# Kernel tuning notes

Hardware: AMD Instinct MI355X
Metric: run time of the kernel (lower is better)

The kernel has to match this reference:

```python
import jax, jax.numpy as jnp
import numpy as np

NIN, NHID, NDECHID, NOUT = 128, 256, 512, 10
B, N = 32, 4096


def _linear_params(key, fan_in, fan_out):
    kw, kb = jax.random.split(key)
    bound = 1.0 / np.sqrt(fan_in)
    W = jax.random.uniform(kw, (fan_in, fan_out), jnp.float32, -bound, bound)
    b = jax.random.uniform(kb, (fan_out,), jnp.float32, -bound, bound)
    return W, b


def setup_inputs() -> dict:
    key = jax.random.key(0)
    ks = jax.random.split(key, 7)
    x = jax.random.normal(ks[0], (B, N, NIN), jnp.float32)
    W1, b1 = _linear_params(ks[1], NIN, NHID)
    W2, b2 = _linear_params(ks[2], NHID, NHID)
    W3, b3 = _linear_params(ks[3], NHID, NHID)
    D1, c1 = _linear_params(ks[4], NHID, NDECHID)
    D2, c2 = _linear_params(ks[5], NDECHID, NDECHID)
    D3, c3 = _linear_params(ks[6], NDECHID, NOUT)
    return {"x": x, "W1": W1, "b1": b1, "W2": W2, "b2": b2, "W3": W3, "b3": b3,
            "D1": D1, "c1": c1, "D2": D2, "c2": c2, "D3": D3, "c3": c3}


def reference(x, W1, b1, W2, b2, W3, b3, D1, c1, D2, c2, D3, c3):
    # encoder MLP: Linear-ReLU-Linear-ReLU-Linear, then extra ReLU
    h = jax.nn.relu(x @ W1 + b1)            # [B, N, nhid]
    h = jax.nn.relu(h @ W2 + b2)
    h = jax.nn.relu(h @ W3 + b3)            # fused enc output + F.relu
    # mean_{i,j}(h_i * h_j) over the set == (mean_i h)^2 elementwise (exact identity)
    m = jnp.mean(h, axis=1)                  # [B, nhid]
    p = jax.nn.relu(m * m)                   # [B, nhid]
    # decoder MLP
    d = jax.nn.relu(p @ D1 + c1)
    d = jax.nn.relu(d @ D2 + c2)
    return d @ D3 + c3                       # [B, nout]
```

## Files before the change

kernel.cpp:

```cpp
#include <hip/hip_runtime.h>
#include <hip/hip_bf16.h>
#include <stdint.h>


#define NIN   128
#define NHID  256
#define NDEC  512
#define NOUTC 10
#define BATCH 32
#define NTOK  4096
#define MTILE 64
#define NBLK  (BATCH * (NTOK / MTILE))

#define SWZ(t) (((t) & 7) << 4)

typedef short bf16x8 __attribute__((ext_vector_type(8)));
typedef float floatx4 __attribute__((ext_vector_type(4)));

__device__ __forceinline__ uint16_t f2b(float f) {
  union { uint32_t u; float f; } v; v.f = f;
  uint32_t r = v.u + 0x7FFFu + ((v.u >> 16) & 1u);
  return (uint16_t)(r >> 16);
}
__device__ __forceinline__ uint32_t pkbf(float lo, float hi) {
  __hip_bfloat162 h = __float22bfloat162_rn(float2{lo, hi});
  union { __hip_bfloat162 h; uint32_t u; } c; c.h = h;
  return c.u;
}

__global__ __launch_bounds__(256) void pack_weights(
    const float* __restrict__ W1, const float* __restrict__ W2,
    const float* __restrict__ W3, const float* __restrict__ c3,
    uint8_t* __restrict__ pW, float* __restrict__ msum,
    float* __restrict__ out) {
  int p = blockIdx.x * blockDim.x + threadIdx.x;
  if (p < BATCH * NHID) msum[p] = 0.f;
  if (p < BATCH * NOUTC) out[p] = c3[p % NOUTC];
  if (p < 32768) {
    int j = p & 7, ln = (p >> 3) & 63, rest = p >> 9;
    int kc = rest & 3, mt = rest >> 2;
    int m = mt * 16 + (ln & 15);
    int k = kc * 32 + ((ln >> 4) << 3) + j;
    ((uint16_t*)pW)[p] = f2b(W1[k * NHID + m]);
  } else {
    int p2 = p - 32768;
    const float* W = (p2 < 65536) ? W2 : W3;
    int base = (p2 < 65536) ? 65536 : 131072;
    if (p2 >= 65536) p2 -= 65536;
    int j = p2 & 7, ln = (p2 >> 3) & 63, rest = p2 >> 9;
    int kc = rest & 7, mt = rest >> 3;
    int m = mt * 16 + (ln & 15);
    int k = kc * 32 + ((ln >> 4) << 3) + j;
    int r = __builtin_amdgcn_cvt_pk_fp8_f32(W[k * NHID + m], 0.f, 0, false);
    pW[base + p2] = (uint8_t)(r & 0xFF);
  }
}

__global__ __launch_bounds__(512) void encoder(
    const float* __restrict__ x,
    const uint8_t* __restrict__ pW,
    const float* __restrict__ b1,
    const float* __restrict__ b2,
    const float* __restrict__ b3,
    float* __restrict__ msum) {
  __shared__ __align__(16) uint8_t Hs[MTILE * 256];
  __shared__ __align__(16) float scr[NHID];

  const int tid  = threadIdx.x;
  const int wave = tid >> 6;
  const int lane = tid & 63;
  const int l15  = lane & 15;
  const int q    = lane >> 4;
  const int tok0  = blockIdx.x * MTILE;
  const int batch = blockIdx.x >> 6;

  const uint16_t* pW1 = (const uint16_t*)pW;
  const uint8_t*  pW2 = pW + 65536;
  const uint8_t*  pW3 = pW + 131072;

  {
    const float4* xv = (const float4*)(x + (size_t)tok0 * NIN);
#pragma unroll
    for (int i = 0; i < 2; ++i) {
      const int u = tid + i * 512;
      float4 va = xv[2 * u];
      float4 vb = xv[2 * u + 1];
      uint4 w = make_uint4(pkbf(va.x, va.y), pkbf(va.z, va.w),
                           pkbf(vb.x, vb.y), pkbf(vb.z, vb.w));
      const int row = u >> 4;
      const int cb  = (u & 15) << 4;
      *(uint4*)&Hs[row * 256 + (cb ^ SWZ(row))] = w;
    }
  }
  __syncthreads();

  floatx4 acc[2][4];

#pragma unroll
  for (int jt = 0; jt < 2; ++jt) {
    const float4 bb = *(const float4*)&b1[(wave * 2 + jt) * 16 + q * 4];
#pragma unroll
    for (int tt = 0; tt < 4; ++tt)
      acc[jt][tt] = (floatx4){bb.x, bb.y, bb.z, bb.w};
  }
#pragma unroll
  for (int kc = 0; kc < 4; ++kc) {
    bf16x8 a0 = *(const bf16x8*)(pW1 + ((((wave * 2 + 0) * 4 + kc) * 64 + lane) << 3));
    bf16x8 a1 = *(const bf16x8*)(pW1 + ((((wave * 2 + 1) * 4 + kc) * 64 + lane) << 3));
#pragma unroll
    for (int tt = 0; tt < 4; ++tt) {
      const int t = tt * 16 + l15;
      bf16x8 b = *(const bf16x8*)&Hs[t * 256 + ((kc * 64 + q * 16) ^ SWZ(t))];
      acc[0][tt] = __builtin_amdgcn_mfma_f32_16x16x32_bf16(a0, b, acc[0][tt], 0, 0, 0);
      acc[1][tt] = __builtin_amdgcn_mfma_f32_16x16x32_bf16(a1, b, acc[1][tt], 0, 0, 0);
    }
  }
  __syncthreads();

#pragma unroll
  for (int jt = 0; jt < 2; ++jt) {
    const int j0 = (wave * 2 + jt) * 16 + q * 4;
#pragma unroll
    for (int tt = 0; tt < 4; ++tt) {
      const int t = tt * 16 + l15;
      float v0 = fmaxf(acc[jt][tt][0], 0.f);
      float v1 = fmaxf(acc[jt][tt][1], 0.f);
      float v2 = fmaxf(acc[jt][tt][2], 0.f);
      float v3 = fmaxf(acc[jt][tt][3], 0.f);
      int u = __builtin_amdgcn_cvt_pk_fp8_f32(v0, v1, 0, false);
      u = __builtin_amdgcn_cvt_pk_fp8_f32(v2, v3, u, true);
      *(uint32_t*)&Hs[t * 256 + (j0 ^ SWZ(t))] = (uint32_t)u;
    }
  }
  __syncthreads();

#pragma unroll
  for (int jt = 0; jt < 2; ++jt) {
    const float4 bb = *(const float4*)&b2[(wave * 2 + jt) * 16 + q * 4];
#pragma unroll
    for (int tt = 0; tt < 4; ++tt)
      acc[jt][tt] = (floatx4){bb.x, bb.y, bb.z, bb.w};
  }
#pragma unroll
  for (int kc = 0; kc < 8; ++kc) {
    long a0 = *(const long*)(pW2 + ((((wave * 2 + 0) * 8 + kc) * 64 + lane) << 3));
    long a1 = *(const long*)(pW2 + ((((wave * 2 + 1) * 8 + kc) * 64 + lane) << 3));
#pragma unroll
    for (int tt = 0; tt < 4; ++tt) {
      const int t = tt * 16 + l15;
      long b = *(const long*)&Hs[t * 256 + ((kc * 32 + q * 8) ^ SWZ(t))];
      acc[0][tt] = __builtin_amdgcn_mfma_f32_16x16x32_fp8_fp8(a0, b, acc[0][tt], 0, 0, 0);
      acc[1][tt] = __builtin_amdgcn_mfma_f32_16x16x32_fp8_fp8(a1, b, acc[1][tt], 0, 0, 0);
    }
  }
  __syncthreads();

#pragma unroll
  for (int jt = 0; jt < 2; ++jt) {
    const int j0 = (wave * 2 + jt) * 16 + q * 4;
#pragma unroll
    for (int tt = 0; tt < 4; ++tt) {
      const int t = tt * 16 + l15;
      float v0 = fmaxf(acc[jt][tt][0], 0.f);
      float v1 = fmaxf(acc[jt][tt][1], 0.f);
      float v2 = fmaxf(acc[jt][tt][2], 0.f);
      float v3 = fmaxf(acc[jt][tt][3], 0.f);
      int u = __builtin_amdgcn_cvt_pk_fp8_f32(v0, v1, 0, false);
      u = __builtin_amdgcn_cvt_pk_fp8_f32(v2, v3, u, true);
      *(uint32_t*)&Hs[t * 256 + (j0 ^ SWZ(t))] = (uint32_t)u;
    }
  }
  __syncthreads();

#pragma unroll
  for (int jt = 0; jt < 2; ++jt) {
    const float4 bb = *(const float4*)&b3[(wave * 2 + jt) * 16 + q * 4];
#pragma unroll
    for (int tt = 0; tt < 4; ++tt)
      acc[jt][tt] = (floatx4){bb.x, bb.y, bb.z, bb.w};
  }
#pragma unroll
  for (int kc = 0; kc < 8; ++kc) {
    long a0 = *(const long*)(pW3 + ((((wave * 2 + 0) * 8 + kc) * 64 + lane) << 3));
    long a1 = *(const long*)(pW3 + ((((wave * 2 + 1) * 8 + kc) * 64 + lane) << 3));
#pragma unroll
    for (int tt = 0; tt < 4; ++tt) {
      const int t = tt * 16 + l15;
      long b = *(const long*)&Hs[t * 256 + ((kc * 32 + q * 8) ^ SWZ(t))];
      acc[0][tt] = __builtin_amdgcn_mfma_f32_16x16x32_fp8_fp8(a0, b, acc[0][tt], 0, 0, 0);
      acc[1][tt] = __builtin_amdgcn_mfma_f32_16x16x32_fp8_fp8(a1, b, acc[1][tt], 0, 0, 0);
    }
  }

#pragma unroll
  for (int jt = 0; jt < 2; ++jt) {
    float s0 = 0.f, s1 = 0.f, s2 = 0.f, s3 = 0.f;
#pragma unroll
    for (int tt = 0; tt < 4; ++tt) {
      s0 += fmaxf(acc[jt][tt][0], 0.f);
      s1 += fmaxf(acc[jt][tt][1], 0.f);
      s2 += fmaxf(acc[jt][tt][2], 0.f);
      s3 += fmaxf(acc[jt][tt][3], 0.f);
    }
#pragma unroll
    for (int m = 1; m <= 8; m <<= 1) {
      s0 += __shfl_xor(s0, m);
      s1 += __shfl_xor(s1, m);
      s2 += __shfl_xor(s2, m);
      s3 += __shfl_xor(s3, m);
    }
    if (l15 == 0)
      *(float4*)&scr[(wave * 2 + jt) * 16 + q * 4] = (float4){s0, s1, s2, s3};
  }
  __syncthreads();
  if (tid < NHID)
    atomicAdd(&msum[batch * NHID + tid], scr[tid]);
}

__global__ __launch_bounds__(1024) void decoder(
    const float* __restrict__ msum,
    const float* __restrict__ D1, const float* __restrict__ c1,
    const float* __restrict__ D2, const float* __restrict__ c2,
    const float* __restrict__ D3,
    float* __restrict__ out) {
  __shared__ float p[NHID];
  __shared__ float d1[NDEC];
  __shared__ float d2q[128];
  __shared__ __align__(16) float red[4096];
  const int b = blockIdx.x >> 2, qd = blockIdx.x & 3, t = threadIdx.x;

  if (t < NHID) {
    float m = msum[b * NHID + t] * (1.f / NTOK);
    p[t] = m * m;
  }
  __syncthreads();

  {
    const int jg = t & 127;
    const int ks = t >> 7;
    const float4* D1v = (const float4*)D1;
    float4 s = {0.f, 0.f, 0.f, 0.f};
    for (int k = ks * 32; k < ks * 32 + 32; ++k) {
      float4 w = D1v[k * 128 + jg];
      float pv = p[k];
      s.x += pv * w.x; s.y += pv * w.y; s.z += pv * w.z; s.w += pv * w.w;
    }
    *(float4*)&red[t * 4] = s;
    __syncthreads();
    if (t < NDEC) {
      float v = c1[t];
#pragma unroll
      for (int i = 0; i < 8; ++i) v += red[i * 512 + t];
      d1[t] = fmaxf(v, 0.f);
    }
    __syncthreads();
  }

  {
    const int jg2 = t & 31;
    const int ks2 = t >> 5;
    const float4* D2v = (const float4*)D2;
    float4 s = {0.f, 0.f, 0.f, 0.f};
    for (int k = ks2 * 16; k < ks2 * 16 + 16; ++k) {
      float4 w = D2v[k * 128 + qd * 32 + jg2];
      float hv = d1[k];
      s.x += hv * w.x; s.y += hv * w.y; s.z += hv * w.z; s.w += hv * w.w;
    }
    *(float4*)&red[t * 4] = s;
    __syncthreads();
    if (t < 128) {
      float v = c2[qd * 128 + t];
#pragma unroll
      for (int i = 0; i < 32; ++i) v += red[i * 128 + t];
      d2q[t] = fmaxf(v, 0.f);
    }
    __syncthreads();
  }

  {
    const int j3 = t & 15;
    const int kc = t >> 4;
    float s = 0.f;
    if (j3 < NOUTC)
      for (int k = kc * 2; k < kc * 2 + 2; ++k)
        s += d2q[k] * D3[(qd * 128 + k) * NOUTC + j3];
    red[t] = s;
    __syncthreads();
    if (t < NOUTC) {
      float v = 0.f;
#pragma unroll
      for (int i = 0; i < 64; ++i) v += red[i * 16 + t];
      atomicAdd(&out[b * NOUTC + t], v);
    }
  }
}

extern "C" void kernel_launch(void* const* d_in, const int* in_sizes, int n_in,
                              void* d_out, int out_size, void* d_ws, size_t ws_size,
                              hipStream_t stream) {
  const float* x  = (const float*)d_in[0];
  const float* W1 = (const float*)d_in[1];
  const float* b1 = (const float*)d_in[2];
  const float* W2 = (const float*)d_in[3];
  const float* b2 = (const float*)d_in[4];
  const float* W3 = (const float*)d_in[5];
  const float* b3 = (const float*)d_in[6];
  const float* D1 = (const float*)d_in[7];
  const float* c1 = (const float*)d_in[8];
  const float* D2 = (const float*)d_in[9];
  const float* c2 = (const float*)d_in[10];
  const float* D3 = (const float*)d_in[11];
  const float* c3 = (const float*)d_in[12];

  uint8_t* pW   = (uint8_t*)d_ws;
  float*   msum = (float*)((char*)d_ws + 384 * 1024);

  pack_weights<<<640, 256, 0, stream>>>(W1, W2, W3, c3, pW, msum,
                                        (float*)d_out);
  encoder<<<NBLK, 512, 0, stream>>>(x, pW, b1, b2, b3, msum);
  decoder<<<128, 1024, 0, stream>>>(msum, D1, c1, D2, c2, D3,
                                    (float*)d_out);
}
```

Baseline: 157.9 us.

## Double-buffer activation tiles and permute fp8 layout for 16-byte LDS reads

Splits the shared activation buffer into two ping-pong buffers so each layer writes its output into the buffer not being read, which lets one __syncthreads per layer transition be removed. The fp8 activations are also stored in a permuted column order with a wider XOR swizzle, so each lane fetches two k-chunks with one 16-byte LDS load instead of two 8-byte loads. This doubles the LDS footprint per block, which may reduce occupancy, and correctness depends on the permuted layout matching the MFMA k ordering.

Result: no change. 155.1 us (-1.7%).

```diff
diff --git a/kernel.cpp b/kernel.cpp
--- a/kernel.cpp
+++ b/kernel.cpp
@@ -12,10 +12,11 @@
 #define MTILE 64
 #define NBLK  (BATCH * (NTOK / MTILE))
 
-#define SWZ(t) (((t) & 7) << 4)
+#define SW2(t) (((t) & 15) << 4)
 
 typedef short bf16x8 __attribute__((ext_vector_type(8)));
 typedef float floatx4 __attribute__((ext_vector_type(4)));
+typedef long  longx2  __attribute__((ext_vector_type(2)));
 
 __device__ __forceinline__ uint16_t f2b(float f) {
   union { uint32_t u; float f; } v; v.f = f;
@@ -63,7 +64,8 @@
     const float* __restrict__ b2,
     const float* __restrict__ b3,
     float* __restrict__ msum) {
-  __shared__ __align__(16) uint8_t Hs[MTILE * 256];
+  __shared__ __align__(16) uint8_t Hs0[MTILE * 256];
+  __shared__ __align__(16) uint8_t Hs1[MTILE * 256];
   __shared__ __align__(16) float scr[NHID];
 
   const int tid  = threadIdx.x;
@@ -89,7 +91,7 @@
                            pkbf(vb.x, vb.y), pkbf(vb.z, vb.w));
       const int row = u >> 4;
       const int cb  = (u & 15) << 4;
-      *(uint4*)&Hs[row * 256 + (cb ^ SWZ(row))] = w;
+      *(uint4*)&Hs0[row * 256 + (cb ^ SW2(row))] = w;
     }
   }
   __syncthreads();
@@ -110,16 +112,15 @@
 #pragma unroll
     for (int tt = 0; tt < 4; ++tt) {
       const int t = tt * 16 + l15;
-      bf16x8 b = *(const bf16x8*)&Hs[t * 256 + ((kc * 64 + q * 16) ^ SWZ(t))];
+      bf16x8 b = *(const bf16x8*)&Hs0[t * 256 + ((kc * 64 + q * 16) ^ SW2(t))];
       acc[0][tt] = __builtin_amdgcn_mfma_f32_16x16x32_bf16(a0, b, acc[0][tt], 0, 0, 0);
       acc[1][tt] = __builtin_amdgcn_mfma_f32_16x16x32_bf16(a1, b, acc[1][tt], 0, 0, 0);
     }
   }
-  __syncthreads();
-
 #pragma unroll
   for (int jt = 0; jt < 2; ++jt) {
     const int j0 = (wave * 2 + jt) * 16 + q * 4;
+    const int pb = ((j0 >> 3) & 3) * 64 + (j0 >> 5) * 8 + (j0 & 7);
 #pragma unroll
     for (int tt = 0; tt < 4; ++tt) {
       const int t = tt * 16 + l15;
@@ -129,7 +130,7 @@
       float v3 = fmaxf(acc[jt][tt][3], 0.f);
       int u = __builtin_amdgcn_cvt_pk_fp8_f32(v0, v1, 0, false);
       u = __builtin_amdgcn_cvt_pk_fp8_f32(v2, v3, u, true);
-      *(uint32_t*)&Hs[t * 256 + (j0 ^ SWZ(t))] = (uint32_t)u;
+      *(uint32_t*)&Hs1[t * 256 + (pb ^ SW2(t))] = (uint32_t)u;
     }
   }
   __syncthreads();
@@ -142,22 +143,29 @@
       acc[jt][tt] = (floatx4){bb.x, bb.y, bb.z, bb.w};
   }
 #pragma unroll
-  for (int kc = 0; kc < 8; ++kc) {
-    long a0 = *(const long*)(pW2 + ((((wave * 2 + 0) * 8 + kc) * 64 + lane) << 3));
-    long a1 = *(const long*)(pW2 + ((((wave * 2 + 1) * 8 + kc) * 64 + lane) << 3));
-#pragma unroll
-    for (int tt = 0; tt < 4; ++tt) {
-      const int t = tt * 16 + l15;
-      long b = *(const long*)&Hs[t * 256 + ((kc * 32 + q * 8) ^ SWZ(t))];
-      acc[0][tt] = __builtin_amdgcn_mfma_f32_16x16x32_fp8_fp8(a0, b, acc[0][tt], 0, 0, 0);
-      acc[1][tt] = __builtin_amdgcn_mfma_f32_16x16x32_fp8_fp8(a1, b, acc[1][tt], 0, 0, 0);
-    }
-  }
-  __syncthreads();
-
+  for (int kc2 = 0; kc2 < 4; ++kc2) {
+    longx2 b[4];
+#pragma unroll
+    for (int tt = 0; tt < 4; ++tt) {
+      const int t = tt * 16 + l15;
+      b[tt] = *(const longx2*)&Hs1[t * 256 + ((q * 64 + kc2 * 16) ^ SW2(t))];
+    }
+#pragma unroll
+    for (int s = 0; s < 2; ++s) {
+      const int kc = kc2 * 2 + s;
+      long a0 = *(const long*)(pW2 + ((((wave * 2 + 0) * 8 + kc) * 64 + lane) << 3));
+      long a1 = *(const long*)(pW2 + ((((wave * 2 + 1) * 8 + kc) * 64 + lane) << 3));
+#pragma unroll
+      for (int tt = 0; tt < 4; ++tt) {
+        acc[0][tt] = __builtin_amdgcn_mfma_f32_16x16x32_fp8_fp8(a0, b[tt][s], acc[0][tt], 0, 0, 0);
+        acc[1][tt] = __builtin_amdgcn_mfma_f32_16x16x32_fp8_fp8(a1, b[tt][s], acc[1][tt], 0, 0, 0);
+      }
+    }
+  }
 #pragma unroll
   for (int jt = 0; jt < 2; ++jt) {
     const int j0 = (wave * 2 + jt) * 16 + q * 4;
+    const int pb = ((j0 >> 3) & 3) * 64 + (j0 >> 5) * 8 + (j0 & 7);
 #pragma unroll
     for (int tt = 0; tt < 4; ++tt) {
       const int t = tt * 16 + l15;
@@ -167,7 +175,7 @@
       float v3 = fmaxf(acc[jt][tt][3], 0.f);
       int u = __builtin_amdgcn_cvt_pk_fp8_f32(v0, v1, 0, false);
       u = __builtin_amdgcn_cvt_pk_fp8_f32(v2, v3, u, true);
-      *(uint32_t*)&Hs[t * 256 + (j0 ^ SWZ(t))] = (uint32_t)u;
+      *(uint32_t*)&Hs0[t * 256 + (pb ^ SW2(t))] = (uint32_t)u;
     }
   }
   __syncthreads();
@@ -180,15 +188,23 @@
       acc[jt][tt] = (floatx4){bb.x, bb.y, bb.z, bb.w};
   }
 #pragma unroll
-  for (int kc = 0; kc < 8; ++kc) {
-    long a0 = *(const long*)(pW3 + ((((wave * 2 + 0) * 8 + kc) * 64 + lane) << 3));
-    long a1 = *(const long*)(pW3 + ((((wave * 2 + 1) * 8 + kc) * 64 + lane) << 3));
-#pragma unroll
-    for (int tt = 0; tt < 4; ++tt) {
-      const int t = tt * 16 + l15;
-      long b = *(const long*)&Hs[t * 256 + ((kc * 32 + q * 8) ^ SWZ(t))];
-      acc[0][tt] = __builtin_amdgcn_mfma_f32_16x16x32_fp8_fp8(a0, b, acc[0][tt], 0, 0, 0);
-      acc[1][tt] = __builtin_amdgcn_mfma_f32_16x16x32_fp8_fp8(a1, b, acc[1][tt], 0, 0, 0);
+  for (int kc2 = 0; kc2 < 4; ++kc2) {
+    longx2 b[4];
+#pragma unroll
+    for (int tt = 0; tt < 4; ++tt) {
+      const int t = tt * 16 + l15;
+      b[tt] = *(const longx2*)&Hs0[t * 256 + ((q * 64 + kc2 * 16) ^ SW2(t))];
+    }
+#pragma unroll
+    for (int s = 0; s < 2; ++s) {
+      const int kc = kc2 * 2 + s;
+      long a0 = *(const long*)(pW3 + ((((wave * 2 + 0) * 8 + kc) * 64 + lane) << 3));
+      long a1 = *(const long*)(pW3 + ((((wave * 2 + 1) * 8 + kc) * 64 + lane) << 3));
+#pragma unroll
+      for (int tt = 0; tt < 4; ++tt) {
+        acc[0][tt] = __builtin_amdgcn_mfma_f32_16x16x32_fp8_fp8(a0, b[tt][s], acc[0][tt], 0, 0, 0);
+        acc[1][tt] = __builtin_amdgcn_mfma_f32_16x16x32_fp8_fp8(a1, b[tt][s], acc[1][tt], 0, 0, 0);
+      }
     }
   }
 
```
